# Kernel optimization log

Hardware: AMD Instinct MI355X
Metric: run time of the kernel (lower is better)

## Reference

```python
import jax, jax.numpy as jnp
import numpy as np

B, S, D, H, F = 2, 2048, 768, 12, 3072
DH = D // H  # head dim = 64


def setup_inputs() -> dict:
    key = jax.random.key(0)
    ks = jax.random.split(key, 16)
    sc = 0.02
    p = {
        "src": jax.random.normal(ks[0], (B, S, D), jnp.float32),
        # attention projections (torch Linear layout: [out, in], bias=True in xformers MultiHeadDispatch)
        "wq": jax.random.normal(ks[1], (D, D), jnp.float32) * sc,
        "bq": jnp.zeros((D,), jnp.float32),
        "wk": jax.random.normal(ks[2], (D, D), jnp.float32) * sc,
        "bk": jnp.zeros((D,), jnp.float32),
        "wv": jax.random.normal(ks[3], (D, D), jnp.float32) * sc,
        "bv": jnp.zeros((D,), jnp.float32),
        "wo": jax.random.normal(ks[4], (D, D), jnp.float32) * sc,
        "bo": jnp.zeros((D,), jnp.float32),
        # FFN: fc1 (bias) -> SwiGLU (two bias-free F->F projections) -> fc2 (bias)
        "w_fc1": jax.random.normal(ks[5], (F, D), jnp.float32) * sc,
        "b_fc1": jnp.zeros((F,), jnp.float32),
        "w_in": jax.random.normal(ks[6], (F, F), jnp.float32) * sc,
        "w_gate": jax.random.normal(ks[7], (F, F), jnp.float32) * sc,
        "w_fc2": jax.random.normal(ks[8], (D, F), jnp.float32) * sc,
        "b_fc2": jnp.zeros((D,), jnp.float32),
        # RMSNorm weights
        "g_attn": jnp.ones((D,), jnp.float32),
        "g_ffn": jnp.ones((D,), jnp.float32),
    }
    return p


def _rmsnorm(x, g):
    eps = jnp.asarray(jnp.finfo(x.dtype).eps, x.dtype)
    return x * jax.lax.rsqrt(jnp.mean(x * x, axis=-1, keepdims=True) + eps) * g


def _rope_cos_sin(seq_len, dim, dtype):
    # xformers RotaryEmbedding: inv_freq over even indices, emb = cat(freqs, freqs)
    inv_freq = 1.0 / (10000.0 ** (jnp.arange(0, dim, 2, dtype=jnp.float32) / dim))
    freqs = jnp.arange(seq_len, dtype=jnp.float32)[:, None] * inv_freq[None, :]  # [S, dim/2]
    emb = jnp.concatenate([freqs, freqs], axis=-1)  # [S, dim]
    return jnp.cos(emb).astype(dtype), jnp.sin(emb).astype(dtype)


def _rotate_half(x):
    x1, x2 = jnp.split(x, 2, axis=-1)
    return jnp.concatenate([-x2, x1], axis=-1)


def _apply_rope(x, cos, sin):
    # x: [B, H, S, DH]; cos/sin: [S, DH]
    return x * cos[None, None] + _rotate_half(x) * sin[None, None]


def _block(src, wq, bq, wk, bk, wv, bv, wo, bo,
           w_fc1, b_fc1, w_in, w_gate, w_fc2, b_fc2, g_attn, g_ffn):
    b, s, d = src.shape
    x = _rmsnorm(src, g_attn)
    q = (x @ wq.T + bq).reshape(b, s, H, DH).transpose(0, 2, 1, 3)
    k = (x @ wk.T + bk).reshape(b, s, H, DH).transpose(0, 2, 1, 3)
    v = (x @ wv.T + bv).reshape(b, s, H, DH).transpose(0, 2, 1, 3)
    cos, sin = _rope_cos_sin(s, DH, x.dtype)
    q = _apply_rope(q, cos, sin)
    k = _apply_rope(k, cos, sin)
    scale = 1.0 / np.sqrt(DH)
    scores = jnp.einsum("bhsd,bhtd->bhst", q * scale, k)  # non-causal, no mask
    attn = jax.nn.softmax(scores, axis=-1)
    ctx = jnp.einsum("bhst,bhtd->bhsd", attn, v)
    ctx = ctx.transpose(0, 2, 1, 3).reshape(b, s, d)
    attn_out = ctx @ wo.T + bo

    y = _rmsnorm(src + attn_out, g_ffn)
    h = y @ w_fc1.T + b_fc1
    h = (h @ w_in.T) * jax.nn.silu(h @ w_gate.T)  # SwiGLU
    ffn_out = h @ w_fc2.T + b_fc2
    return y + ffn_out


def reference(src, wq, bq, wk, bk, wv, bv, wo, bo,
              w_fc1, b_fc1, w_in, w_gate, w_fc2, b_fc2, g_attn, g_ffn):
    return _block(src, wq, bq, wk, bk, wv, bv, wo, bo,
                  w_fc1, b_fc1, w_in, w_gate, w_fc2, b_fc2, g_attn, g_ffn)
```

## Files before the change

kernel.cpp:

```cpp
#include <hip/hip_runtime.h>

#define DEV static __device__ __forceinline__

typedef __attribute__((ext_vector_type(8))) short bf16x8;
typedef __attribute__((ext_vector_type(4))) short short4v;
typedef __attribute__((ext_vector_type(4))) float f32x4;

DEV f32x4 mfma16(bf16x8 a, bf16x8 b, f32x4 c){
  return __builtin_amdgcn_mfma_f32_16x16x32_bf16(a, b, c, 0, 0, 0);
}
DEV float bf2f(short s){ union{unsigned u; float f;} v; v.u=((unsigned)(unsigned short)s)<<16; return v.f; }
DEV short f2bf(float f){ union{float f; unsigned u;} v; v.f=f; unsigned r=v.u+0x7fffu+((v.u>>16)&1u); return (short)(r>>16); }
DEV void gload16(const void* g, void* l){
  __builtin_amdgcn_global_load_lds((const __attribute__((address_space(1))) void*)g,
                                   (__attribute__((address_space(3))) void*)l, 16, 0, 0);
}
DEV int cvtpk(float lo, float hi){
  int r; asm("v_cvt_pk_bf16_f32 %0, %1, %2" : "=v"(r) : "v"(lo), "v"(hi)); return r;
}

enum { EPI_QKV=4 };

__global__ void k_fatD(const float* __restrict__ p0, const float* __restrict__ p1,
                       const float* __restrict__ p2, const float* __restrict__ p3,
                       short* __restrict__ dst,
                       const float* __restrict__ x, const float* __restrict__ g,
                       short* __restrict__ out){
  const int id = blockIdx.x;
  const int tid = threadIdx.x;
  if (id < 2304){
    int v = id*256 + tid;
    const float* src; int rel;
    if      (v < 147456){ src=p0; rel=v; }
    else if (v < 294912){ src=p1; rel=v-147456; }
    else if (v < 442368){ src=p2; rel=v-294912; }
    else                { src=p3; rel=v-442368; }
    float4 xv = ((const float4*)src)[rel];
    short4v o; o.x=f2bf(xv.x); o.y=f2bf(xv.y); o.z=f2bf(xv.z); o.w=f2bf(xv.w);
    ((short4v*)dst)[v] = o;
  } else {
    int row = (id-2304)*4 + (tid>>6);
    int lane = tid & 63;
    const float* xr = x + (size_t)row*768;
    float4 v[3];
    float ss = 0.f;
    #pragma unroll
    for (int i=0;i<3;i++){
      v[i] = *(const float4*)(xr + i*256 + lane*4);
      ss += v[i].x*v[i].x + v[i].y*v[i].y + v[i].z*v[i].z + v[i].w*v[i].w;
    }
    #pragma unroll
    for (int d=32; d>0; d>>=1) ss += __shfl_xor(ss, d);
    float sc = rsqrtf(ss*(1.f/768.f) + 1.1920929e-7f);
    #pragma unroll
    for (int i=0;i<3;i++){
      int c0 = i*256 + lane*4;
      float4 gv = *(const float4*)(g + c0);
      short4v o;
      o.x = f2bf(v[i].x*sc*gv.x); o.y = f2bf(v[i].y*sc*gv.y);
      o.z = f2bf(v[i].z*sc*gv.z); o.w = f2bf(v[i].w*sc*gv.w);
      *(short4v*)(out + (size_t)row*768 + c0) = o;
    }
  }
}

template<int EPI>
__launch_bounds__(256, 2)
__global__ void k_gemm(const short* __restrict__ Aptr, const short* __restrict__ Bptr,
                       void* __restrict__ Cout, const float* __restrict__ bias,
                       const void* __restrict__ aux, const float* __restrict__ bias2,
                       const float* __restrict__ bias3, const void* __restrict__ aux2,
                       int M, int N, int K){
  __shared__ short ldsA[128*32];
  __shared__ short ldsB[128*32];
  const int t = threadIdx.x;
  const int wave = t >> 6, lane = t & 63;
  const int l15 = lane & 15, l4 = lane >> 4;
  const int nwg = gridDim.x * gridDim.y;
  const int bid0 = blockIdx.y * gridDim.x + blockIdx.x;
  const int cpx = nwg >> 3;
  const int bid = (bid0 & 7) * cpx + (bid0 >> 3);
  const int bm = bid / gridDim.x, bn = bid % gridDim.x;
  const int wr = wave >> 1, wc = wave & 1;

  f32x4 acc[4][4] = {};

  const short* Ag = Aptr + (size_t)(bm*128 + wave*32 + (lane>>2))*K + (lane&3)*8;
  const short* Bg = Bptr + (size_t)(bn*128 + wave*32 + (lane>>2))*K + (lane&3)*8;
  short* lA = ldsA + wave*1024;
  short* lB = ldsB + wave*1024;

  for (int k0 = 0; k0 < K; k0 += 32){
    __syncthreads();
    gload16(Ag + k0,                lA);
    gload16(Ag + k0 + 16*(size_t)K, lA + 512);
    gload16(Bg + k0,                lB);
    gload16(Bg + k0 + 16*(size_t)K, lB + 512);
    __syncthreads();
    bf16x8 af[4], bfr[4];
    #pragma unroll
    for (int m=0;m<4;m++) af[m]  = *(const bf16x8*)(ldsA + (wr*64 + m*16 + l15)*32 + l4*8);
    #pragma unroll
    for (int n=0;n<4;n++) bfr[n] = *(const bf16x8*)(ldsB + (wc*64 + n*16 + l15)*32 + l4*8);
    #pragma unroll
    for (int m=0;m<4;m++)
      #pragma unroll
      for (int n=0;n<4;n++)
        acc[m][n] = mfma16(af[m], bfr[n], acc[m][n]);
  }

  const int row0 = bm*128 + wr*64;
  const int col0 = bn*128 + wc*64;

  if constexpr (EPI == EPI_QKV){
    const int proj = col0 / 768;
    const int c768 = col0 - proj*768;
    const int h = c768 >> 6;
    const float* bs = proj==0 ? bias : (proj==1 ? bias2 : bias3);
    float bvv[4];
    #pragma unroll
    for (int n=0;n<4;n++) bvv[n] = bs[c768 + n*16 + l15];
    if (proj == 2){
      short* Ov = (short*)const_cast<void*>(aux2);
      #pragma unroll
      for (int m=0;m<4;m++){
        int s0 = row0 + m*16 + l4*4;
        int b = s0 >> 11, s = s0 & 2047;
        size_t hb = (size_t)(b*12 + h)*64;
        #pragma unroll
        for (int n=0;n<4;n++){
          short4v pk;
          pk.x = f2bf(acc[m][n][0] + bvv[n]);
          pk.y = f2bf(acc[m][n][1] + bvv[n]);
          pk.z = f2bf(acc[m][n][2] + bvv[n]);
          pk.w = f2bf(acc[m][n][3] + bvv[n]);
          *(short4v*)(Ov + (hb + n*16 + l15)*2048 + s) = pk;
        }
      }
    } else {
      short* O = proj==0 ? (short*)Cout : (short*)const_cast<void*>(aux);
      const float sc = proj==0 ? 0.18033688011112042f : 1.0f;
      const float RC = 0.41524101186092034f;
      float invf0 = exp2f(-(float)l15 * RC);
      float invf1 = exp2f(-(float)(16 + l15) * RC);
      #pragma unroll
      for (int m=0;m<4;m++){
        #pragma unroll
        for (int j=0;j<4;j++){
          int row = row0 + m*16 + l4*4 + j;
          int b = row >> 11, s = row & 2047;
          size_t obase = ((size_t)(b*12 + h)*2048 + (size_t)s)*64;
          float a0 = acc[m][0][j] + bvv[0];
          float a1 = acc[m][1][j] + bvv[1];
          float a2 = acc[m][2][j] + bvv[2];
          float a3 = acc[m][3][j] + bvv[3];
          float sn0, cs0, sn1, cs1;
          __sincosf((float)s * invf0, &sn0, &cs0);
          __sincosf((float)s * invf1, &sn1, &cs1);
          O[obase + l15]      = f2bf((a0*cs0 - a2*sn0)*sc);
          O[obase + 16 + l15] = f2bf((a1*cs1 - a3*sn1)*sc);
          O[obase + 32 + l15] = f2bf((a2*cs0 + a0*sn0)*sc);
          O[obase + 48 + l15] = f2bf((a3*cs1 + a1*sn1)*sc);
        }
      }
    }
  }
}

__launch_bounds__(256, 5)
__global__ void k_fatA(const short* __restrict__ Q, const short* __restrict__ Kb,
                       const short* __restrict__ Vb, short* __restrict__ ctx,
                       const float* __restrict__ winf, const float* __restrict__ wgf,
                       const float* __restrict__ wfc2f, short* __restrict__ dstbig,
                       const float* __restrict__ wfc1, short* __restrict__ wfc1T){
  __shared__ short shm[16384];
  const int id = blockIdx.x;
  const int tid = threadIdx.x;

  if (id < 768){
    const int wave = tid>>6, lane = tid&63;
    const int l15 = lane&15, l4 = lane>>4;
    const int qt = id & 31, bh = id >> 5;
    const short* Qh  = Q  + (size_t)bh*2048*64;
    const short* Kh  = Kb + (size_t)bh*2048*64;
    const short* Vth = Vb + (size_t)bh*64*2048;

    const int r7  = lane>>3;
    const int swz = ((lane&7) ^ r7) << 3;
    const int rr0 = wave*8 + r7, rr1 = 32 + wave*8 + r7;
    const size_t kOff0 = (size_t)rr0*64   + swz, kOff1 = (size_t)rr1*64   + swz;
    const size_t vOff0 = (size_t)rr0*2048 + swz, vOff1 = (size_t)rr1*2048 + swz;

    bf16x8 qf[2];
    #pragma unroll
    for (int kf=0;kf<2;kf++)
      qf[kf] = *(const bf16x8*)(Qh + (size_t)(qt*64 + wave*16 + l15)*64 + kf*32 + l4*8);

    f32x4 cacc[4] = {};
    f32x4 lacc = {};
    union { int w[4]; bf16x8 v; } onesf;
    onesf.w[0] = onesf.w[1] = onesf.w[2] = onesf.w[3] = 0x3F803F80;

    #define STAGE(sel, kv0) do { \
      const short* ksp = Kh + (size_t)(kv0)*64; \
      const short* vsp = Vth + (kv0); \
      short* kd = shm + (sel)*4096 + wave*512; \
      short* vd = shm + 8192 + (sel)*4096 + wave*512; \
      gload16(ksp + kOff0, kd); \
      gload16(ksp + kOff1, kd + 2048); \
      gload16(vsp + vOff0, vd); \
      gload16(vsp + vOff1, vd + 2048); \
    } while(0)

    STAGE(0, 0);

    for (int tt = 0; tt < 32; ++tt){
      const int cur = tt & 1;
      if (tt < 31){
        STAGE(cur^1, (tt+1)*64);
        asm volatile("s_waitcnt vmcnt(4)" ::: "memory");
      } else {
        asm volatile("s_waitcnt vmcnt(0)" ::: "memory");
      }
      __builtin_amdgcn_sched_barrier(0);
      __builtin_amdgcn_s_barrier();
      __builtin_amdgcn_sched_barrier(0);

      const short* KtC = shm + cur*4096;
      const short* VtC = shm + 8192 + cur*4096;

      f32x4 sacc[4] = {};
      __builtin_amdgcn_s_setprio(1);
      #pragma unroll
      for (int kf=0;kf<2;kf++){
        #pragma unroll
        for (int mk=0;mk<4;mk++){
          int r = mk*16 + l15;
          bf16x8 kfr = *(const bf16x8*)(KtC + r*64 + (((kf*4+l4) ^ (l15&7))<<3));
          sacc[mk] = mfma16(kfr, qf[kf], sacc[mk]);
        }
      }
      __builtin_amdgcn_s_setprio(0);

      int pk01[4], pk23[4];
      #pragma unroll
      for (int mk=0;mk<4;mk++){
        float p0 = exp2f(sacc[mk][0]);
        float p1 = exp2f(sacc[mk][1]);
        float p2 = exp2f(sacc[mk][2]);
        float p3 = exp2f(sacc[mk][3]);
        pk01[mk] = cvtpk(p0, p1);
        pk23[mk] = cvtpk(p2, p3);
      }

      #pragma unroll
      for (int ks=0;ks<2;ks++){
        int srcA = l15 + ((l4&1)<<5);
        int srcB = srcA + 16;
        int hi = l4>>1;
        int w0a = __shfl(pk01[2*ks], srcA), w0b = __shfl(pk01[2*ks+1], srcA);
        int w1a = __shfl(pk23[2*ks], srcA), w1b = __shfl(pk23[2*ks+1], srcA);
        int w2a = __shfl(pk01[2*ks], srcB), w2b = __shfl(pk01[2*ks+1], srcB);
        int w3a = __shfl(pk23[2*ks], srcB), w3b = __shfl(pk23[2*ks+1], srcB);
        union { int w[4]; bf16x8 v; } pa;
        pa.w[0] = hi ? w0b : w0a;
        pa.w[1] = hi ? w1b : w1a;
        pa.w[2] = hi ? w2b : w2a;
        pa.w[3] = hi ? w3b : w3a;
        __builtin_amdgcn_s_setprio(1);
        #pragma unroll
        for (int nf=0;nf<4;nf++){
          int dh = nf*16 + l15;
          bf16x8 vf = *(const bf16x8*)(VtC + dh*64 + (((ks*4+l4) ^ (dh&7))<<3));
          cacc[nf] = mfma16(pa.v, vf, cacc[nf]);
        }
        lacc = mfma16(pa.v, onesf.v, lacc);
        __builtin_amdgcn_s_setprio(0);
      }

      __builtin_amdgcn_sched_barrier(0);
      __builtin_amdgcn_s_barrier();
    }
    #undef STAGE

    const int b = bh/12, h = bh%12;
    #pragma unroll
    for (int j=0;j<4;j++){
      float inv = 1.f / lacc[j];
      int s = qt*64 + wave*16 + l4*4 + j;
      size_t base = ((size_t)b*2048 + s)*768 + h*64;
      #pragma unroll
      for (int nf=0;nf<4;nf++)
        ctx[base + nf*16 + l15] = f2bf(cacc[nf][j] * inv);
    }
  } else if (id < 21504){
    int v = (id - 768)*256 + tid;
    const float* src; int rel;
    if      (v < 2359296){ src=winf;  rel=v; }
    else if (v < 4718592){ src=wgf;   rel=v-2359296; }
    else                 { src=wfc2f; rel=v-4718592; }
    float4 x = ((const float4*)src)[rel];
    short4v o; o.x=f2bf(x.x); o.y=f2bf(x.y); o.z=f2bf(x.z); o.w=f2bf(x.w);
    ((short4v*)dstbig)[v] = o;
  } else {
    int idx = id - 21504;
    int f0 = (idx % 96)*32, d0 = (idx / 96)*32;
    float* lt = (float*)shm;
    int r = tid >> 3, c4 = tid & 7;
    float4 v = *(const float4*)(wfc1 + (size_t)(f0 + r)*768 + d0 + c4*4);
    lt[r*33 + c4*4+0] = v.x; lt[r*33 + c4*4+1] = v.y;
    lt[r*33 + c4*4+2] = v.z; lt[r*33 + c4*4+3] = v.w;
    __syncthreads();
    short4v o;
    o.x = f2bf(lt[(c4*4+0)*33 + r]);
    o.y = f2bf(lt[(c4*4+1)*33 + r]);
    o.z = f2bf(lt[(c4*4+2)*33 + r]);
    o.w = f2bf(lt[(c4*4+3)*33 + r]);
    *(short4v*)(wfc1T + (size_t)(d0 + r)*3072 + f0 + c4*4) = o;
  }
}

__launch_bounds__(256, 2)
__global__ void k_fatB(const short* __restrict__ ctxb, const short* __restrict__ wo_b,
                       float* __restrict__ resid, const float* __restrict__ bo,
                       const float* __restrict__ srcf,
                       const short* __restrict__ win_b, const short* __restrict__ wfc1T,
                       short* __restrict__ Pw,
                       const float* __restrict__ bfc1, float* __restrict__ bvg){
  __shared__ short shm[8192];
  const int id = blockIdx.x;
  const int t = threadIdx.x;
  const int wave = t >> 6, lane = t & 63;
  const int l15 = lane & 15, l4 = lane >> 4;
  const int wr = wave >> 1, wc = wave & 1;
  short* lA = shm + wave*1024;
  short* lB = shm + 4096 + wave*1024;

  if (id < 192){
    const int bid = (id & 7)*24 + (id >> 3);
    const int bm = bid / 6, bn = bid % 6;
    f32x4 acc[4][4] = {};
    const short* Ag = ctxb + (size_t)(bm*128 + wave*32 + (lane>>2))*768 + (lane&3)*8;
    const short* Bg = wo_b + (size_t)(bn*128 + wave*32 + (lane>>2))*768 + (lane&3)*8;
    for (int k0 = 0; k0 < 768; k0 += 32){
      __syncthreads();
      gload16(Ag + k0,          lA);
      gload16(Ag + k0 + 16*768, lA + 512);
      gload16(Bg + k0,          lB);
      gload16(Bg + k0 + 16*768, lB + 512);
      __syncthreads();
      bf16x8 af[4], bfr[4];
      #pragma unroll
      for (int m=0;m<4;m++) af[m]  = *(const bf16x8*)(shm + (wr*64 + m*16 + l15)*32 + l4*8);
      #pragma unroll
      for (int n=0;n<4;n++) bfr[n] = *(const bf16x8*)(shm + 4096 + (wc*64 + n*16 + l15)*32 + l4*8);
      #pragma unroll
      for (int m=0;m<4;m++)
        #pragma unroll
        for (int n=0;n<4;n++)
          acc[m][n] = mfma16(af[m], bfr[n], acc[m][n]);
    }
    const int row0 = bm*128 + wr*64;
    const int col0 = bn*128 + wc*64;
    float bvv[4];
    #pragma unroll
    for (int n=0;n<4;n++) bvv[n] = bo[col0 + n*16 + l15];
    #pragma unroll
    for (int m=0;m<4;m++)
      #pragma unroll
      for (int j=0;j<4;j++){
        size_t rb = (size_t)(row0 + m*16 + l4*4 + j)*768 + col0 + l15;
        #pragma unroll
        for (int n=0;n<4;n++) resid[rb + n*16] = acc[m][n][j] + bvv[n] + srcf[rb + n*16];
      }
  } else if (id < 768){
    const int id2 = id - 192;
    const int z = id2 / 288;
    const int rest = id2 - z*288;
    const int koff = z * 1536;
    const int bid = (rest & 7)*36 + (rest >> 3);
    const int bm = bid / 6, bn = bid % 6;
    f32x4 acc[4][4] = {};
    const short* Ag = win_b + (size_t)(bm*128 + wave*32 + (lane>>2))*3072 + (lane&3)*8 + koff;
    const short* Bg = wfc1T + (size_t)(bn*128 + wave*32 + (lane>>2))*3072 + (lane&3)*8 + koff;
    for (int k0 = 0; k0 < 1536; k0 += 32){
      __syncthreads();
      gload16(Ag + k0,           lA);
      gload16(Ag + k0 + 16*3072, lA + 512);
      gload16(Bg + k0,           lB);
      gload16(Bg + k0 + 16*3072, lB + 512);
      __syncthreads();
      bf16x8 af[4], bfr[4];
      #pragma unroll
      for (int m=0;m<4;m++) af[m]  = *(const bf16x8*)(shm + (wr*64 + m*16 + l15)*32 + l4*8);
      #pragma unroll
      for (int n=0;n<4;n++) bfr[n] = *(const bf16x8*)(shm + 4096 + (wc*64 + n*16 + l15)*32 + l4*8);
      #pragma unroll
      for (int m=0;m<4;m++)
        #pragma unroll
        for (int n=0;n<4;n++)
          acc[m][n] = mfma16(af[m], bfr[n], acc[m][n]);
    }
    short* Pz = Pw + (size_t)z * 4718592;
    const int row0 = bm*128 + wr*64;
    const int col0 = bn*128 + wc*64;
    #pragma unroll
    for (int m=0;m<4;m++)
      #pragma unroll
      for (int j=0;j<4;j++){
        size_t rb = (size_t)(row0 + m*16 + l4*4 + j)*768 + col0 + l15;
        #pragma unroll
        for (int n=0;n<4;n++) Pz[rb + n*16] = f2bf(acc[m][n][j]);
      }
  } else {
    int row = (id - 768)*4 + wave;
    const short* wrow = win_b + (size_t)row*3072 + lane*48;
    const float* bb = bfc1 + lane*48;
    float s = 0.f;
    #pragma unroll
    for (int i=0;i<6;i++){
      bf16x8 w = *(const bf16x8*)(wrow + i*8);
      float4 b0 = *(const float4*)(bb + i*8);
      float4 b1 = *(const float4*)(bb + i*8 + 4);
      s += bf2f(w[0])*b0.x + bf2f(w[1])*b0.y + bf2f(w[2])*b0.z + bf2f(w[3])*b0.w
         + bf2f(w[4])*b1.x + bf2f(w[5])*b1.y + bf2f(w[6])*b1.z + bf2f(w[7])*b1.w;
    }
    #pragma unroll
    for (int d=32; d>0; d>>=1) s += __shfl_xor(s, d);
    if (lane == 0) bvg[row] = s;
  }
}

__global__ void k_fatC(const float* __restrict__ resid, const float* __restrict__ gffn,
                       short* __restrict__ yb,
                       const short* __restrict__ Pw, short* __restrict__ comp){
  const int id = blockIdx.x;
  if (id < 1024){
    int row = id*4 + (threadIdx.x>>6);
    int lane = threadIdx.x & 63;
    const float* xr = resid + (size_t)row*768;
    float4 v[3];
    float ss = 0.f;
    #pragma unroll
    for (int i=0;i<3;i++){
      v[i] = *(const float4*)(xr + i*256 + lane*4);
      ss += v[i].x*v[i].x + v[i].y*v[i].y + v[i].z*v[i].z + v[i].w*v[i].w;
    }
    #pragma unroll
    for (int d=32; d>0; d>>=1) ss += __shfl_xor(ss, d);
    float sc = rsqrtf(ss*(1.f/768.f) + 1.1920929e-7f);
    #pragma unroll
    for (int i=0;i<3;i++){
      int c0 = i*256 + lane*4;
      float4 gv = *(const float4*)(gffn + c0);
      short4v o;
      o.x = f2bf(v[i].x*sc*gv.x); o.y = f2bf(v[i].y*sc*gv.y);
      o.z = f2bf(v[i].z*sc*gv.z); o.w = f2bf(v[i].w*sc*gv.w);
      *(short4v*)(yb + (size_t)row*768 + c0) = o;
    }
  } else {
    int i = (id - 1024)*256 + threadIdx.x;
    short4v a = ((const short4v*)Pw)[i];
    short4v b = ((const short4v*)(Pw + 4718592))[i];
    short4v o;
    o.x = f2bf(bf2f(a.x) + bf2f(b.x)); o.y = f2bf(bf2f(a.y) + bf2f(b.y));
    o.z = f2bf(bf2f(a.z) + bf2f(b.z)); o.w = f2bf(bf2f(a.w) + bf2f(b.w));
    ((short4v*)comp)[i] = o;
  }
}

__launch_bounds__(256, 2)
__global__ void k_part(const short* __restrict__ Aptr, const short* __restrict__ Bptr,
                       short* __restrict__ Pa, short* __restrict__ Pb){
  __shared__ short ldsA[128*32];
  __shared__ short ldsB[128*32];
  const int t = threadIdx.x;
  const int wave = t >> 6, lane = t & 63;
  const int l15 = lane & 15, l4 = lane >> 4;
  const int K = 3072;
  const int z = blockIdx.z;
  const int koff = z * 768;
  const int bid0 = blockIdx.y * 6 + blockIdx.x;
  const int bid = (bid0 & 7) * 24 + (bid0 >> 3);
  const int bm = bid / 6, bn = bid % 6;
  const int wr = wave >> 1, wc = wave & 1;

  f32x4 acc[4][4] = {};

  const short* Ag = Aptr + (size_t)(bm*128 + wave*32 + (lane>>2))*K + (lane&3)*8 + koff;
  const short* Bg = Bptr + (size_t)(bn*128 + wave*32 + (lane>>2))*K + (lane&3)*8 + koff;
  short* lA = ldsA + wave*1024;
  short* lB = ldsB + wave*1024;

  for (int k0 = 0; k0 < 768; k0 += 32){
    __syncthreads();
    gload16(Ag + k0,                lA);
    gload16(Ag + k0 + 16*(size_t)K, lA + 512);
    gload16(Bg + k0,                lB);
    gload16(Bg + k0 + 16*(size_t)K, lB + 512);
    __syncthreads();
    bf16x8 af[4], bfr[4];
    #pragma unroll
    for (int m=0;m<4;m++) af[m]  = *(const bf16x8*)(ldsA + (wr*64 + m*16 + l15)*32 + l4*8);
    #pragma unroll
    for (int n=0;n<4;n++) bfr[n] = *(const bf16x8*)(ldsB + (wc*64 + n*16 + l15)*32 + l4*8);
    #pragma unroll
    for (int m=0;m<4;m++)
      #pragma unroll
      for (int n=0;n<4;n++)
        acc[m][n] = mfma16(af[m], bfr[n], acc[m][n]);
  }

  short* P = (z < 2) ? (Pa + (size_t)z*3145728) : (Pb + (size_t)(z-2)*3145728);
  const int row0 = bm*128 + wr*64;
  const int col0 = bn*128 + wc*64;
  #pragma unroll
  for (int m=0;m<4;m++)
    #pragma unroll
    for (int j=0;j<4;j++){
      size_t rb = (size_t)(row0 + m*16 + l4*4 + j)*768 + col0 + l15;
      #pragma unroll
      for (int n=0;n<4;n++) P[rb + n*16] = f2bf(acc[m][n][j]);
    }
}

__global__ void k_fc2red(const short* __restrict__ Pa, const short* __restrict__ Pb,
                         const float* __restrict__ bias, const short* __restrict__ yv,
                         float* __restrict__ out){
  int i = blockIdx.x * 256 + threadIdx.x;
  short4v a = ((const short4v*)Pa)[i];
  short4v b = ((const short4v*)(Pa + 3145728))[i];
  short4v c = ((const short4v*)Pb)[i];
  short4v d = ((const short4v*)(Pb + 3145728))[i];
  float4 bv = *(const float4*)(bias + (i % 192)*4);
  short4v y = ((const short4v*)yv)[i];
  float4 o;
  o.x = bf2f(a.x) + bf2f(b.x) + bf2f(c.x) + bf2f(d.x) + bv.x + bf2f(y.x);
  o.y = bf2f(a.y) + bf2f(b.y) + bf2f(c.y) + bf2f(d.y) + bv.y + bf2f(y.y);
  o.z = bf2f(a.z) + bf2f(b.z) + bf2f(c.z) + bf2f(d.z) + bv.z + bf2f(y.z);
  o.w = bf2f(a.w) + bf2f(b.w) + bf2f(c.w) + bf2f(d.w) + bv.w + bf2f(y.w);
  ((float4*)out)[i] = o;
}

__launch_bounds__(256, 2)
__global__ void k_ffglu(const short* __restrict__ Aptr, const short* __restrict__ Wcomp,
                        const float* __restrict__ bvg, short* __restrict__ Cout){
  __shared__ short lds[3*12288];
  const int tid = threadIdx.x;
  const int wave = tid >> 6, lane = tid & 63;
  const int l15 = lane & 15, l4 = lane >> 4;
  const int wm = wave >> 1, wn = wave & 1;
  const int K = 768, N = 3072;
  const int nt = 24;

  const int lin = blockIdx.y * 48 + blockIdx.x;
  const int xcd = lin & 7, idx = lin >> 3;
  const int bm = ((xcd & 1) << 3) + idx / 12;
  const int bn = (xcd >> 1) * 12 + idx % 12;

  const int srcC = ((lane & 3) ^ ((lane >> 3) & 3)) * 8;

  const short* aSrc[4];
  int aDst[4];
  #pragma unroll
  for (int i=0;i<4;i++){
    int s = i*4 + wave;
    int row = s*16 + (lane>>2);
    aSrc[i] = Aptr + (size_t)(bm*256 + row)*K + srcC;
    aDst[i] = s*512;
  }
  const short* bSrc[2];
  int bDst[2];
  #pragma unroll
  for (int i=0;i<2;i++){
    int j = i*4 + wave;
    int pidx = (j>>1)*16 + (lane>>2);
    int grow = (j & 1) ? 3072 : 0;
    bSrc[i] = Wcomp + (size_t)(grow + bn*64 + pidx)*K + srcC;
    bDst[i] = 8192 + j*512;
  }

  int offA[8], offB[4];
  #pragma unroll
  for (int m=0;m<8;m++){
    int r = wm*128 + m*16 + l15;
    offA[m] = r*32 + ((l4 ^ ((l15>>1)&3))<<3);
  }
  #pragma unroll
  for (int nf=0;nf<4;nf++){
    int r = wn*64 + nf*16 + l15;
    offB[nf] = 8192 + r*32 + ((l4 ^ ((l15>>1)&3))<<3);
  }

  f32x4 accv[8][2] = {};
  f32x4 accg[8][2] = {};

  short *b0 = lds, *b1 = lds + 12288, *b2 = lds + 24576;

  #define GSTAGE_ALL(buf, t) do{ \
    gload16(aSrc[0] + (size_t)(t)*32, (buf) + aDst[0]); \
    gload16(aSrc[1] + (size_t)(t)*32, (buf) + aDst[1]); \
    gload16(aSrc[2] + (size_t)(t)*32, (buf) + aDst[2]); \
    gload16(aSrc[3] + (size_t)(t)*32, (buf) + aDst[3]); \
    gload16(bSrc[0] + (size_t)(t)*32, (buf) + bDst[0]); \
    gload16(bSrc[1] + (size_t)(t)*32, (buf) + bDst[1]); \
  }while(0)

  GSTAGE_ALL(b0, 0);
  GSTAGE_ALL(b1, 1);

  for (int t = 0; t < nt; ++t){
    if (t < nt-1){
      asm volatile("s_waitcnt vmcnt(6)" ::: "memory");
    } else {
      asm volatile("s_waitcnt vmcnt(0)" ::: "memory");
    }
    __builtin_amdgcn_sched_barrier(0);
    __builtin_amdgcn_s_barrier();
    __builtin_amdgcn_sched_barrier(0);

    if (t + 2 < nt) GSTAGE_ALL(b2, t+2);

    bf16x8 a0 = *(const bf16x8*)(b0 + offA[0]);
    bf16x8 a1 = *(const bf16x8*)(b0 + offA[1]);
    bf16x8 a2 = *(const bf16x8*)(b0 + offA[2]);
    bf16x8 a3 = *(const bf16x8*)(b0 + offA[3]);
    bf16x8 a4 = *(const bf16x8*)(b0 + offA[4]);
    bf16x8 a5 = *(const bf16x8*)(b0 + offA[5]);
    bf16x8 a6 = *(const bf16x8*)(b0 + offA[6]);
    bf16x8 a7 = *(const bf16x8*)(b0 + offA[7]);
    bf16x8 v0 = *(const bf16x8*)(b0 + offB[0]);
    bf16x8 g0 = *(const bf16x8*)(b0 + offB[1]);
    bf16x8 v1 = *(const bf16x8*)(b0 + offB[2]);
    bf16x8 g1 = *(const bf16x8*)(b0 + offB[3]);

    __builtin_amdgcn_s_setprio(1);
    accv[0][0] = mfma16(a0, v0, accv[0][0]);  accg[0][0] = mfma16(a0, g0, accg[0][0]);
    accv[1][0] = mfma16(a1, v0, accv[1][0]);  accg[1][0] = mfma16(a1, g0, accg[1][0]);
    accv[2][0] = mfma16(a2, v0, accv[2][0]);  accg[2][0] = mfma16(a2, g0, accg[2][0]);
    accv[3][0] = mfma16(a3, v0, accv[3][0]);  accg[3][0] = mfma16(a3, g0, accg[3][0]);
    accv[0][1] = mfma16(a0, v1, accv[0][1]);  accg[0][1] = mfma16(a0, g1, accg[0][1]);
    accv[1][1] = mfma16(a1, v1, accv[1][1]);  accg[1][1] = mfma16(a1, g1, accg[1][1]);
    accv[2][1] = mfma16(a2, v1, accv[2][1]);  accg[2][1] = mfma16(a2, g1, accg[2][1]);
    accv[3][1] = mfma16(a3, v1, accv[3][1]);  accg[3][1] = mfma16(a3, g1, accg[3][1]);
    accv[4][0] = mfma16(a4, v0, accv[4][0]);  accg[4][0] = mfma16(a4, g0, accg[4][0]);
    accv[5][0] = mfma16(a5, v0, accv[5][0]);  accg[5][0] = mfma16(a5, g0, accg[5][0]);
    accv[6][0] = mfma16(a6, v0, accv[6][0]);  accg[6][0] = mfma16(a6, g0, accg[6][0]);
    accv[7][0] = mfma16(a7, v0, accv[7][0]);  accg[7][0] = mfma16(a7, g0, accg[7][0]);
    accv[4][1] = mfma16(a4, v1, accv[4][1]);  accg[4][1] = mfma16(a4, g1, accg[4][1]);
    accv[5][1] = mfma16(a5, v1, accv[5][1]);  accg[5][1] = mfma16(a5, g1, accg[5][1]);
    accv[6][1] = mfma16(a6, v1, accv[6][1]);  accg[6][1] = mfma16(a6, g1, accg[6][1]);
    accv[7][1] = mfma16(a7, v1, accv[7][1]);  accg[7][1] = mfma16(a7, g1, accg[7][1]);
    __builtin_amdgcn_s_setprio(0);

    short* tmp = b0; b0 = b1; b1 = b2; b2 = tmp;
  }
  #undef GSTAGE_ALL

  const int row0 = bm*256 + wm*128;
  #pragma unroll
  for (int m=0;m<8;m++){
    #pragma unroll
    for (int j=0;j<4;j++){
      size_t rb = (size_t)(row0 + m*16 + l4*4 + j)*N + bn*64 + wn*32 + l15;
      #pragma unroll
      for (int p=0;p<2;p++){
        int c = bn*64 + wn*32 + p*16 + l15;
        float g = accg[m][p][j] + bvg[3072 + c];
        float v = accv[m][p][j] + bvg[c];
        Cout[rb + p*16] = f2bf(v * g / (1.f + __expf(-g)));
      }
    }
  }
}

extern "C" void kernel_launch(void* const* d_in, const int* in_sizes, int n_in,
                              void* d_out, int out_size, void* d_ws, size_t ws_size,
                              hipStream_t stream){
  (void)in_sizes; (void)n_in; (void)out_size;
  const float* src   = (const float*)d_in[0];
  const float* wq    = (const float*)d_in[1];
  const float* bq    = (const float*)d_in[2];
  const float* wk    = (const float*)d_in[3];
  const float* bk    = (const float*)d_in[4];
  const float* wv    = (const float*)d_in[5];
  const float* bv    = (const float*)d_in[6];
  const float* wo    = (const float*)d_in[7];
  const float* bo    = (const float*)d_in[8];
  const float* wfc1  = (const float*)d_in[9];
  const float* bfc1  = (const float*)d_in[10];
  const float* win   = (const float*)d_in[11];
  const float* wgate = (const float*)d_in[12];
  const float* wfc2  = (const float*)d_in[13];
  const float* bfc2  = (const float*)d_in[14];
  const float* gattn = (const float*)d_in[15];
  const float* gffn  = (const float*)d_in[16];

  char* ws = (char*)d_ws;
  constexpr size_t SZ_W768  = 768ull*768*2;
  constexpr size_t SZ_WFC   = 3072ull*768*2;
  constexpr size_t SZ_WFF   = 3072ull*3072*2;
  constexpr size_t SZ_ACT   = 4096ull*768*2;
  constexpr size_t SZ_ACTF  = 4096ull*768*4;
  constexpr size_t SZ_H     = 4096ull*3072*2;
  constexpr size_t OFF_WQ    = 0;
  constexpr size_t OFF_WK    = OFF_WQ + SZ_W768;
  constexpr size_t OFF_WV    = OFF_WK + SZ_W768;
  constexpr size_t OFF_WO    = OFF_WV + SZ_W768;
  constexpr size_t OFF_WFC1  = OFF_WO + SZ_W768;
  constexpr size_t OFF_WIN   = OFF_WFC1 + SZ_WFC;
  constexpr size_t OFF_WGATE = OFF_WIN + SZ_WFF;
  constexpr size_t OFF_WFC2  = OFF_WGATE + SZ_WFF;
  constexpr size_t OFF_XN    = OFF_WFC2 + SZ_WFC;
  constexpr size_t OFF_Q     = OFF_XN + SZ_ACT;
  constexpr size_t OFF_K     = OFF_Q + SZ_ACT;
  constexpr size_t OFF_V     = OFF_K + SZ_ACT;
  constexpr size_t OFF_RES   = OFF_V + SZ_ACT;
  constexpr size_t OFF_HIN   = OFF_RES + SZ_ACTF;
  constexpr size_t OFF_H2    = OFF_HIN + SZ_H;
  constexpr size_t WS_NEED   = OFF_H2 + SZ_H;
  if (ws_size < WS_NEED) return;

  constexpr size_t OFF_COMP  = OFF_HIN;
  constexpr size_t OFF_T     = OFF_HIN + 6144ull*768*2;
  constexpr size_t OFF_BVG   = OFF_T + 768ull*3072*2;

  short* wq_b    = (short*)(ws+OFF_WQ);
  short* win_b   = (short*)(ws+OFF_WIN);
  short* wfc2_b  = (short*)(ws+OFF_WFC2);
  short* wo_b    = (short*)(ws+OFF_WO);
  short* xn      = (short*)(ws+OFF_XN);
  short* ctxb    = (short*)(ws+OFF_XN);
  short* qb      = (short*)(ws+OFF_Q);
  short* yb      = (short*)(ws+OFF_Q);
  short* kb2     = (short*)(ws+OFF_K);
  short* vb2     = (short*)(ws+OFF_V);
  float* resid   = (float*)(ws+OFF_RES);
  short* comp    = (short*)(ws+OFF_COMP);
  short* wfc1T   = (short*)(ws+OFF_T);
  float* bvg     = (float*)(ws+OFF_BVG);
  short* h2      = (short*)(ws+OFF_H2);
  short* Pw      = (short*)(ws+OFF_H2);
  short* partA   = (short*)(ws+OFF_HIN);
  short* partB   = (short*)(ws+OFF_K);

  k_fatD<<<3328, 256, 0, stream>>>(wq, wk, wv, wo, wq_b, src, gattn, xn);

  k_gemm<EPI_QKV><<<dim3(18,32), 256, 0, stream>>>(xn, wq_b, qb, bq, kb2, bk, bv, vb2, 4096, 2304, 768);

  k_fatA<<<23808, 256, 0, stream>>>(qb, kb2, vb2, ctxb, win, wgate, wfc2, win_b, wfc1, wfc1T);

  k_fatB<<<2304, 256, 0, stream>>>(ctxb, wo_b, resid, bo, src, win_b, wfc1T, Pw, bfc1, bvg);

  k_fatC<<<5632, 256, 0, stream>>>(resid, gffn, yb, Pw, comp);

  k_ffglu<<<dim3(48,16), 256, 0, stream>>>(yb, comp, bvg, h2);

  k_part<<<dim3(6,32,4), 256, 0, stream>>>(h2, wfc2_b, partA, partB);
  k_fc2red<<<3072, 256, 0, stream>>>(partA, partB, bfc2, yb, (float*)d_out);
}
```

Baseline: 233.2 us.

## Double attention query tile per block to reuse K/V tiles across two query groups

The attention part of the fused kernel now processes 128 query rows per block (32 per wave, as two 16-row groups) instead of 64, halving the number of attention blocks. Each K and V fragment loaded from LDS feeds MFMAs for both query groups, so global and LDS K/V traffic per query is halved. The cost is more accumulator registers, reflected in dropping the launch bound from 5 to 2 blocks per CU, and fewer attention blocks to fill the GPU (384). The weight-conversion block offsets are shifted to match.

```diff
diff --git a/kernel.cpp b/kernel.cpp
--- a/kernel.cpp
+++ b/kernel.cpp
@@ -167,7 +167,7 @@
   }
 }
 
-__launch_bounds__(256, 5)
+__launch_bounds__(256, 2)
 __global__ void k_fatA(const short* __restrict__ Q, const short* __restrict__ Kb,
                        const short* __restrict__ Vb, short* __restrict__ ctx,
                        const float* __restrict__ winf, const float* __restrict__ wgf,
@@ -177,10 +177,10 @@
   const int id = blockIdx.x;
   const int tid = threadIdx.x;
 
-  if (id < 768){
+  if (id < 384){
     const int wave = tid>>6, lane = tid&63;
     const int l15 = lane&15, l4 = lane>>4;
-    const int qt = id & 31, bh = id >> 5;
+    const int qt = id & 15, bh = id >> 4;
     const short* Qh  = Q  + (size_t)bh*2048*64;
     const short* Kh  = Kb + (size_t)bh*2048*64;
     const short* Vth = Vb + (size_t)bh*64*2048;
@@ -191,13 +191,15 @@
     const size_t kOff0 = (size_t)rr0*64   + swz, kOff1 = (size_t)rr1*64   + swz;
     const size_t vOff0 = (size_t)rr0*2048 + swz, vOff1 = (size_t)rr1*2048 + swz;
 
-    bf16x8 qf[2];
-    #pragma unroll
-    for (int kf=0;kf<2;kf++)
-      qf[kf] = *(const bf16x8*)(Qh + (size_t)(qt*64 + wave*16 + l15)*64 + kf*32 + l4*8);
-
-    f32x4 cacc[4] = {};
-    f32x4 lacc = {};
+    bf16x8 qf[2][2];
+    #pragma unroll
+    for (int qg=0;qg<2;qg++)
+      #pragma unroll
+      for (int kf=0;kf<2;kf++)
+        qf[qg][kf] = *(const bf16x8*)(Qh + (size_t)(qt*128 + wave*32 + qg*16 + l15)*64 + kf*32 + l4*8);
+
+    f32x4 cacc[2][4] = {};
+    f32x4 lacc[2] = {};
     union { int w[4]; bf16x8 v; } onesf;
     onesf.w[0] = onesf.w[1] = onesf.w[2] = onesf.w[3] = 0x3F803F80;
 
@@ -229,53 +231,67 @@
       const short* KtC = shm + cur*4096;
       const short* VtC = shm + 8192 + cur*4096;
 
-      f32x4 sacc[4] = {};
-      __builtin_amdgcn_s_setprio(1);
+      f32x4 sacc[2][4] = {};
       #pragma unroll
       for (int kf=0;kf<2;kf++){
+        bf16x8 kfr[4];
         #pragma unroll
         for (int mk=0;mk<4;mk++){
           int r = mk*16 + l15;
-          bf16x8 kfr = *(const bf16x8*)(KtC + r*64 + (((kf*4+l4) ^ (l15&7))<<3));
-          sacc[mk] = mfma16(kfr, qf[kf], sacc[mk]);
+          kfr[mk] = *(const bf16x8*)(KtC + r*64 + (((kf*4+l4) ^ (l15&7))<<3));
         }
-      }
-      __builtin_amdgcn_s_setprio(0);
-
-      int pk01[4], pk23[4];
-      #pragma unroll
-      for (int mk=0;mk<4;mk++){
-        float p0 = exp2f(sacc[mk][0]);
-        float p1 = exp2f(sacc[mk][1]);
-        float p2 = exp2f(sacc[mk][2]);
-        float p3 = exp2f(sacc[mk][3]);
-        pk01[mk] = cvtpk(p0, p1);
-        pk23[mk] = cvtpk(p2, p3);
+        __builtin_amdgcn_s_setprio(1);
+        #pragma unroll
+        for (int mk=0;mk<4;mk++){
+          sacc[0][mk] = mfma16(kfr[mk], qf[0][kf], sacc[0][mk]);
+          sacc[1][mk] = mfma16(kfr[mk], qf[1][kf], sacc[1][mk]);
+        }
+        __builtin_amdgcn_s_setprio(0);
+      }
+
+      int pk01[2][4], pk23[2][4];
+      #pragma unroll
+      for (int qg=0;qg<2;qg++){
+        #pragma unroll
+        for (int mk=0;mk<4;mk++){
+          float p0 = exp2f(sacc[qg][mk][0]);
+          float p1 = exp2f(sacc[qg][mk][1]);
+          float p2 = exp2f(sacc[qg][mk][2]);
+          float p3 = exp2f(sacc[qg][mk][3]);
+          pk01[qg][mk] = cvtpk(p0, p1);
+          pk23[qg][mk] = cvtpk(p2, p3);
+        }
       }
 
       #pragma unroll
       for (int ks=0;ks<2;ks++){
-        int srcA = l15 + ((l4&1)<<5);
-        int srcB = srcA + 16;
-        int hi = l4>>1;
-        int w0a = __shfl(pk01[2*ks], srcA), w0b = __shfl(pk01[2*ks+1], srcA);
-        int w1a = __shfl(pk23[2*ks], srcA), w1b = __shfl(pk23[2*ks+1], srcA);
-        int w2a = __shfl(pk01[2*ks], srcB), w2b = __shfl(pk01[2*ks+1], srcB);
-        int w3a = __shfl(pk23[2*ks], srcB), w3b = __shfl(pk23[2*ks+1], srcB);
-        union { int w[4]; bf16x8 v; } pa;
-        pa.w[0] = hi ? w0b : w0a;
-        pa.w[1] = hi ? w1b : w1a;
-        pa.w[2] = hi ? w2b : w2a;
-        pa.w[3] = hi ? w3b : w3a;
-        __builtin_amdgcn_s_setprio(1);
+        bf16x8 vf[4];
         #pragma unroll
         for (int nf=0;nf<4;nf++){
           int dh = nf*16 + l15;
-          bf16x8 vf = *(const bf16x8*)(VtC + dh*64 + (((ks*4+l4) ^ (dh&7))<<3));
-          cacc[nf] = mfma16(pa.v, vf, cacc[nf]);
+          vf[nf] = *(const bf16x8*)(VtC + dh*64 + (((ks*4+l4) ^ (dh&7))<<3));
         }
-        lacc = mfma16(pa.v, onesf.v, lacc);
-        __builtin_amdgcn_s_setprio(0);
+        #pragma unroll
+        for (int qg=0;qg<2;qg++){
+          int srcA = l15 + ((l4&1)<<5);
+          int srcB = srcA + 16;
+          int hi = l4>>1;
+          int w0a = __shfl(pk01[qg][2*ks], srcA), w0b = __shfl(pk01[qg][2*ks+1], srcA);
+          int w1a = __shfl(pk23[qg][2*ks], srcA), w1b = __shfl(pk23[qg][2*ks+1], srcA);
+          int w2a = __shfl(pk01[qg][2*ks], srcB), w2b = __shfl(pk01[qg][2*ks+1], srcB);
+          int w3a = __shfl(pk23[qg][2*ks], srcB), w3b = __shfl(pk23[qg][2*ks+1], srcB);
+          union { int w[4]; bf16x8 v; } pa;
+          pa.w[0] = hi ? w0b : w0a;
+          pa.w[1] = hi ? w1b : w1a;
+          pa.w[2] = hi ? w2b : w2a;
+          pa.w[3] = hi ? w3b : w3a;
+          __builtin_amdgcn_s_setprio(1);
+          #pragma unroll
+          for (int nf=0;nf<4;nf++)
+            cacc[qg][nf] = mfma16(pa.v, vf[nf], cacc[qg][nf]);
+          lacc[qg] = mfma16(pa.v, onesf.v, lacc[qg]);
+          __builtin_amdgcn_s_setprio(0);
+        }
       }
 
       __builtin_amdgcn_sched_barrier(0);
@@ -285,16 +301,19 @@
 
     const int b = bh/12, h = bh%12;
     #pragma unroll
-    for (int j=0;j<4;j++){
-      float inv = 1.f / lacc[j];
-      int s = qt*64 + wave*16 + l4*4 + j;
-      size_t base = ((size_t)b*2048 + s)*768 + h*64;
-      #pragma unroll
-      for (int nf=0;nf<4;nf++)
-        ctx[base + nf*16 + l15] = f2bf(cacc[nf][j] * inv);
-    }
-  } else if (id < 21504){
-    int v = (id - 768)*256 + tid;
+    for (int qg=0;qg<2;qg++){
+      #pragma unroll
+      for (int j=0;j<4;j++){
+        float inv = 1.f / lacc[qg][j];
+        int s = qt*128 + wave*32 + qg*16 + l4*4 + j;
+        size_t base = ((size_t)b*2048 + s)*768 + h*64;
+        #pragma unroll
+        for (int nf=0;nf<4;nf++)
+          ctx[base + nf*16 + l15] = f2bf(cacc[qg][nf][j] * inv);
+      }
+    }
+  } else if (id < 21120){
+    int v = (id - 384)*256 + tid;
     const float* src; int rel;
     if      (v < 2359296){ src=winf;  rel=v; }
     else if (v < 4718592){ src=wgf;   rel=v-2359296; }
@@ -303,7 +322,7 @@
     short4v o; o.x=f2bf(x.x); o.y=f2bf(x.y); o.z=f2bf(x.z); o.w=f2bf(x.w);
     ((short4v*)dstbig)[v] = o;
   } else {
-    int idx = id - 21504;
+    int idx = id - 21120;
     int f0 = (idx % 96)*32, d0 = (idx / 96)*32;
     float* lt = (float*)shm;
     int r = tid >> 3, c4 = tid & 7;
@@ -748,7 +767,7 @@
 
   k_gemm<EPI_QKV><<<dim3(18,32), 256, 0, stream>>>(xn, wq_b, qb, bq, kb2, bk, bv, vb2, 4096, 2304, 768);
 
-  k_fatA<<<23808, 256, 0, stream>>>(qb, kb2, vb2, ctxb, win, wgate, wfc2, win_b, wfc1, wfc1T);
+  k_fatA<<<23424, 256, 0, stream>>>(qb, kb2, vb2, ctxb, win, wgate, wfc2, win_b, wfc1, wfc1T);
 
   k_fatB<<<2304, 256, 0, stream>>>(ctxb, wo_b, resid, bo, src, win_b, wfc1T, Pw, bfc1, bvg);
 
```

Measured after the change: 239.0 us. 2.5% more time.

## Replace QKV GEMM with triple-buffered swizzled 256x64 tile kernel

Applied to the files above, without the earlier changes.

Replaces the generic templated GEMM for the QKV projection with a dedicated kernel. It uses 256x64 tiles aligned to one head per block, a three-stage LDS ring of async global-to-LDS loads with explicit vmcnt waits, and a single barrier per k-step. It also applies an XOR swizzle on LDS columns to avoid bank conflicts and raises MFMA issue priority. The intent is to overlap loads with MFMA and cut barrier stalls, at the cost of more LDS per block and a wider B-tile footprint.

```diff
diff --git a/kernel.cpp b/kernel.cpp
--- a/kernel.cpp
+++ b/kernel.cpp
@@ -18,8 +18,6 @@
 DEV int cvtpk(float lo, float hi){
   int r; asm("v_cvt_pk_bf16_f32 %0, %1, %2" : "=v"(r) : "v"(lo), "v"(hi)); return r;
 }
-
-enum { EPI_QKV=4 };
 
 __global__ void k_fatD(const float* __restrict__ p0, const float* __restrict__ p1,
                        const float* __restrict__ p2, const float* __restrict__ p3,
@@ -64,104 +62,149 @@
   }
 }
 
-template<int EPI>
 __launch_bounds__(256, 2)
-__global__ void k_gemm(const short* __restrict__ Aptr, const short* __restrict__ Bptr,
-                       void* __restrict__ Cout, const float* __restrict__ bias,
-                       const void* __restrict__ aux, const float* __restrict__ bias2,
-                       const float* __restrict__ bias3, const void* __restrict__ aux2,
-                       int M, int N, int K){
-  __shared__ short ldsA[128*32];
-  __shared__ short ldsB[128*32];
-  const int t = threadIdx.x;
-  const int wave = t >> 6, lane = t & 63;
-  const int l15 = lane & 15, l4 = lane >> 4;
-  const int nwg = gridDim.x * gridDim.y;
-  const int bid0 = blockIdx.y * gridDim.x + blockIdx.x;
-  const int cpx = nwg >> 3;
-  const int bid = (bid0 & 7) * cpx + (bid0 >> 3);
-  const int bm = bid / gridDim.x, bn = bid % gridDim.x;
-  const int wr = wave >> 1, wc = wave & 1;
+__global__ void k_qkv(const short* __restrict__ xn, const short* __restrict__ Wqkv,
+                      const float* __restrict__ bq, const float* __restrict__ bk,
+                      const float* __restrict__ bv,
+                      short* __restrict__ Oq, short* __restrict__ Ok, short* __restrict__ Ov){
+  __shared__ short lds[3*10240];
+  const int tid = threadIdx.x;
+  const int wave = tid>>6, lane = tid&63;
+  const int l15 = lane&15, l4 = lane>>4;
+  const int nt = 24;
+
+  const int bid0 = blockIdx.y*36 + blockIdx.x;
+  const int bid = (bid0 & 7)*72 + (bid0>>3);
+  const int bm = bid / 36, bn = bid % 36;
+
+  const int srcC = ((lane&3) ^ ((lane>>3)&3)) * 8;
+
+  const short* sSrc[5];
+  int sDst[5];
+  #pragma unroll
+  for (int i=0;i<5;i++){
+    int s = wave + 4*i;
+    if (s < 16){
+      int row = bm*256 + s*16 + (lane>>2);
+      sSrc[i] = xn + (size_t)row*768 + srcC;
+      sDst[i] = s*512;
+    } else {
+      int row = bn*64 + (s-16)*16 + (lane>>2);
+      sSrc[i] = Wqkv + (size_t)row*768 + srcC;
+      sDst[i] = 8192 + (s-16)*512;
+    }
+  }
+
+  int offA[4], offB[4];
+  #pragma unroll
+  for (int m=0;m<4;m++){
+    int r = wave*64 + m*16 + l15;
+    offA[m] = r*32 + ((l4 ^ ((l15>>1)&3))<<3);
+  }
+  #pragma unroll
+  for (int n=0;n<4;n++){
+    int r = n*16 + l15;
+    offB[n] = 8192 + r*32 + ((l4 ^ ((l15>>1)&3))<<3);
+  }
 
   f32x4 acc[4][4] = {};
-
-  const short* Ag = Aptr + (size_t)(bm*128 + wave*32 + (lane>>2))*K + (lane&3)*8;
-  const short* Bg = Bptr + (size_t)(bn*128 + wave*32 + (lane>>2))*K + (lane&3)*8;
-  short* lA = ldsA + wave*1024;
-  short* lB = ldsB + wave*1024;
-
-  for (int k0 = 0; k0 < K; k0 += 32){
-    __syncthreads();
-    gload16(Ag + k0,                lA);
-    gload16(Ag + k0 + 16*(size_t)K, lA + 512);
-    gload16(Bg + k0,                lB);
-    gload16(Bg + k0 + 16*(size_t)K, lB + 512);
-    __syncthreads();
-    bf16x8 af[4], bfr[4];
-    #pragma unroll
-    for (int m=0;m<4;m++) af[m]  = *(const bf16x8*)(ldsA + (wr*64 + m*16 + l15)*32 + l4*8);
-    #pragma unroll
-    for (int n=0;n<4;n++) bfr[n] = *(const bf16x8*)(ldsB + (wc*64 + n*16 + l15)*32 + l4*8);
-    #pragma unroll
-    for (int m=0;m<4;m++)
-      #pragma unroll
-      for (int n=0;n<4;n++)
-        acc[m][n] = mfma16(af[m], bfr[n], acc[m][n]);
-  }
-
-  const int row0 = bm*128 + wr*64;
-  const int col0 = bn*128 + wc*64;
-
-  if constexpr (EPI == EPI_QKV){
-    const int proj = col0 / 768;
-    const int c768 = col0 - proj*768;
-    const int h = c768 >> 6;
-    const float* bs = proj==0 ? bias : (proj==1 ? bias2 : bias3);
-    float bvv[4];
-    #pragma unroll
-    for (int n=0;n<4;n++) bvv[n] = bs[c768 + n*16 + l15];
-    if (proj == 2){
-      short* Ov = (short*)const_cast<void*>(aux2);
-      #pragma unroll
-      for (int m=0;m<4;m++){
-        int s0 = row0 + m*16 + l4*4;
-        int b = s0 >> 11, s = s0 & 2047;
-        size_t hb = (size_t)(b*12 + h)*64;
-        #pragma unroll
-        for (int n=0;n<4;n++){
-          short4v pk;
-          pk.x = f2bf(acc[m][n][0] + bvv[n]);
-          pk.y = f2bf(acc[m][n][1] + bvv[n]);
-          pk.z = f2bf(acc[m][n][2] + bvv[n]);
-          pk.w = f2bf(acc[m][n][3] + bvv[n]);
-          *(short4v*)(Ov + (hb + n*16 + l15)*2048 + s) = pk;
-        }
+  short *b0 = lds, *b1 = lds + 10240, *b2 = lds + 20480;
+
+  #define QSTAGE(buf, t) do{ \
+    gload16(sSrc[0] + (size_t)(t)*32, (buf) + sDst[0]); \
+    gload16(sSrc[1] + (size_t)(t)*32, (buf) + sDst[1]); \
+    gload16(sSrc[2] + (size_t)(t)*32, (buf) + sDst[2]); \
+    gload16(sSrc[3] + (size_t)(t)*32, (buf) + sDst[3]); \
+    gload16(sSrc[4] + (size_t)(t)*32, (buf) + sDst[4]); \
+  }while(0)
+
+  QSTAGE(b0, 0);
+  QSTAGE(b1, 1);
+
+  for (int t = 0; t < nt; ++t){
+    if (t < nt-1){
+      asm volatile("s_waitcnt vmcnt(5)" ::: "memory");
+    } else {
+      asm volatile("s_waitcnt vmcnt(0)" ::: "memory");
+    }
+    __builtin_amdgcn_sched_barrier(0);
+    __builtin_amdgcn_s_barrier();
+    __builtin_amdgcn_sched_barrier(0);
+
+    if (t + 2 < nt) QSTAGE(b2, t+2);
+
+    bf16x8 a0 = *(const bf16x8*)(b0 + offA[0]);
+    bf16x8 a1 = *(const bf16x8*)(b0 + offA[1]);
+    bf16x8 a2 = *(const bf16x8*)(b0 + offA[2]);
+    bf16x8 a3 = *(const bf16x8*)(b0 + offA[3]);
+    bf16x8 w0 = *(const bf16x8*)(b0 + offB[0]);
+    bf16x8 w1 = *(const bf16x8*)(b0 + offB[1]);
+    bf16x8 w2 = *(const bf16x8*)(b0 + offB[2]);
+    bf16x8 w3 = *(const bf16x8*)(b0 + offB[3]);
+
+    __builtin_amdgcn_s_setprio(1);
+    acc[0][0] = mfma16(a0, w0, acc[0][0]);  acc[0][1] = mfma16(a0, w1, acc[0][1]);
+    acc[1][0] = mfma16(a1, w0, acc[1][0]);  acc[1][1] = mfma16(a1, w1, acc[1][1]);
+    acc[2][0] = mfma16(a2, w0, acc[2][0]);  acc[2][1] = mfma16(a2, w1, acc[2][1]);
+    acc[3][0] = mfma16(a3, w0, acc[3][0]);  acc[3][1] = mfma16(a3, w1, acc[3][1]);
+    acc[0][2] = mfma16(a0, w2, acc[0][2]);  acc[0][3] = mfma16(a0, w3, acc[0][3]);
+    acc[1][2] = mfma16(a1, w2, acc[1][2]);  acc[1][3] = mfma16(a1, w3, acc[1][3]);
+    acc[2][2] = mfma16(a2, w2, acc[2][2]);  acc[2][3] = mfma16(a2, w3, acc[2][3]);
+    acc[3][2] = mfma16(a3, w2, acc[3][2]);  acc[3][3] = mfma16(a3, w3, acc[3][3]);
+    __builtin_amdgcn_s_setprio(0);
+
+    short* tmp = b0; b0 = b1; b1 = b2; b2 = tmp;
+  }
+  #undef QSTAGE
+
+  const int row0 = bm*256 + wave*64;
+  const int proj = bn / 12;
+  const int h = bn % 12;
+  const float* bs = proj==0 ? bq : (proj==1 ? bk : bv);
+  float bvv[4];
+  #pragma unroll
+  for (int n=0;n<4;n++) bvv[n] = bs[h*64 + n*16 + l15];
+
+  if (proj == 2){
+    #pragma unroll
+    for (int m=0;m<4;m++){
+      int s0 = row0 + m*16 + l4*4;
+      int b = s0 >> 11, s = s0 & 2047;
+      size_t hb = (size_t)(b*12 + h)*64;
+      #pragma unroll
+      for (int n=0;n<4;n++){
+        short4v pk;
+        pk.x = f2bf(acc[m][n][0] + bvv[n]);
+        pk.y = f2bf(acc[m][n][1] + bvv[n]);
+        pk.z = f2bf(acc[m][n][2] + bvv[n]);
+        pk.w = f2bf(acc[m][n][3] + bvv[n]);
+        *(short4v*)(Ov + (hb + n*16 + l15)*2048 + s) = pk;
       }
-    } else {
-      short* O = proj==0 ? (short*)Cout : (short*)const_cast<void*>(aux);
-      const float sc = proj==0 ? 0.18033688011112042f : 1.0f;
-      const float RC = 0.41524101186092034f;
-      float invf0 = exp2f(-(float)l15 * RC);
-      float invf1 = exp2f(-(float)(16 + l15) * RC);
-      #pragma unroll
-      for (int m=0;m<4;m++){
-        #pragma unroll
-        for (int j=0;j<4;j++){
-          int row = row0 + m*16 + l4*4 + j;
-          int b = row >> 11, s = row & 2047;
-          size_t obase = ((size_t)(b*12 + h)*2048 + (size_t)s)*64;
-          float a0 = acc[m][0][j] + bvv[0];
-          float a1 = acc[m][1][j] + bvv[1];
-          float a2 = acc[m][2][j] + bvv[2];
-          float a3 = acc[m][3][j] + bvv[3];
-          float sn0, cs0, sn1, cs1;
-          __sincosf((float)s * invf0, &sn0, &cs0);
-          __sincosf((float)s * invf1, &sn1, &cs1);
-          O[obase + l15]      = f2bf((a0*cs0 - a2*sn0)*sc);
-          O[obase + 16 + l15] = f2bf((a1*cs1 - a3*sn1)*sc);
-          O[obase + 32 + l15] = f2bf((a2*cs0 + a0*sn0)*sc);
-          O[obase + 48 + l15] = f2bf((a3*cs1 + a1*sn1)*sc);
-        }
+    }
+  } else {
+    short* O = proj==0 ? Oq : Ok;
+    const float sc = proj==0 ? 0.18033688011112042f : 1.0f;
+    const float RC = 0.41524101186092034f;
+    float invf0 = exp2f(-(float)l15 * RC);
+    float invf1 = exp2f(-(float)(16 + l15) * RC);
+    #pragma unroll
+    for (int m=0;m<4;m++){
+      #pragma unroll
+      for (int j=0;j<4;j++){
+        int row = row0 + m*16 + l4*4 + j;
+        int b = row >> 11, s = row & 2047;
+        size_t obase = ((size_t)(b*12 + h)*2048 + (size_t)s)*64;
+        float a0 = acc[m][0][j] + bvv[0];
+        float a1 = acc[m][1][j] + bvv[1];
+        float a2 = acc[m][2][j] + bvv[2];
+        float a3 = acc[m][3][j] + bvv[3];
+        float sn0, cs0, sn1, cs1;
+        __sincosf((float)s * invf0, &sn0, &cs0);
+        __sincosf((float)s * invf1, &sn1, &cs1);
+        O[obase + l15]      = f2bf((a0*cs0 - a2*sn0)*sc);
+        O[obase + 16 + l15] = f2bf((a1*cs1 - a3*sn1)*sc);
+        O[obase + 32 + l15] = f2bf((a2*cs0 + a0*sn0)*sc);
+        O[obase + 48 + l15] = f2bf((a3*cs1 + a1*sn1)*sc);
       }
     }
   }
@@ -746,7 +789,7 @@
 
   k_fatD<<<3328, 256, 0, stream>>>(wq, wk, wv, wo, wq_b, src, gattn, xn);
 
-  k_gemm<EPI_QKV><<<dim3(18,32), 256, 0, stream>>>(xn, wq_b, qb, bq, kb2, bk, bv, vb2, 4096, 2304, 768);
+  k_qkv<<<dim3(36,16), 256, 0, stream>>>(xn, wq_b, bq, bk, bv, qb, kb2, vb2);
 
   k_fatA<<<23808, 256, 0, stream>>>(qb, kb2, vb2, ctxb, win, wgate, wfc2, win_b, wfc1, wfc1T);
 
```

New measurement: 241.8 us. 3.7% more time.
